# Kernel optimization log

Measured on AMD Instinct MI355X. Metric: run time of the kernel, lower is better.

## Reference

```python
import jax, jax.numpy as jnp
import numpy as np

HEADS = 4  # from init_kwargs

def setup_inputs() -> dict:
    key = jax.random.key(0)
    ks = jax.random.split(key, 11)
    B, N, T, E = 1, 16, 2048, 64
    D = E // HEADS
    return {
        "value": jax.random.normal(ks[0], (B, N, T, E), jnp.float32),
        "key":   jax.random.normal(ks[1], (B, N, T, E), jnp.float32),
        "query": jax.random.normal(ks[2], (B, N, T, E), jnp.float32),
        "Wq": jax.random.normal(ks[3], (D, D), jnp.float32) / np.sqrt(D),
        "bq": jax.random.normal(ks[4], (D,), jnp.float32) * 0.01,
        "Wk": jax.random.normal(ks[5], (D, D), jnp.float32) / np.sqrt(D),
        "bk": jax.random.normal(ks[6], (D,), jnp.float32) * 0.01,
        "Wv": jax.random.normal(ks[7], (D, D), jnp.float32) / np.sqrt(D),
        "bv": jax.random.normal(ks[8], (D,), jnp.float32) * 0.01,
        "Wfc": jax.random.normal(ks[9], (E, E), jnp.float32) / np.sqrt(E),
        "bfc": jax.random.normal(ks[10], (E,), jnp.float32) * 0.01,
    }

def reference(value, key, query, Wq, bq, Wk, bk, Wv, bv, Wfc, bfc):
    B, N, T, E = query.shape
    H = HEADS
    D = E // H
    # split heads: [B,N,T,H,D]
    q = query.reshape(B, N, T, H, D) @ Wq + bq
    k = key.reshape(B, N, T, H, D) @ Wk + bk
    v = value.reshape(B, N, T, H, D) @ Wv + bv
    # full score tensor [B,N,Tq,Tk,H]
    scores = jnp.einsum('bnqhd,bnkhd->bnqkh', q, k)
    # NOTE: original softmaxes over dim=2, i.e. the QUERY axis (faithful to source)
    attn = jax.nn.softmax(scores / jnp.float32(E) ** 0.5, axis=2)
    out = jnp.einsum('bnqkh,bnkhd->bnqhd', attn, v).reshape(B, N, T, E)
    return out @ Wfc + bfc
```

## Files before the change

kernel.cpp:

```cpp
#include <hip/hip_runtime.h>

#define N_ 16
#define T_ 2048
#define E_ 64
#define H_ 4
#define D_ 16
#define NH_ 64
#define SEXP_ 0.18033688f

typedef __attribute__((ext_vector_type(4))) _Float16 h4;
typedef __attribute__((ext_vector_type(8))) _Float16 h8;
typedef __attribute__((ext_vector_type(2))) __fp16 g2;
typedef __attribute__((ext_vector_type(4))) float f4;

#if __has_builtin(__builtin_amdgcn_exp2f)
__device__ inline float fast_exp2(float x) { return __builtin_amdgcn_exp2f(x); }
#else
__device__ inline float fast_exp2(float x) {
    float r; asm("v_exp_f32 %0, %1" : "=v"(r) : "v"(x)); return r;
}
#endif

#if __has_builtin(__builtin_amdgcn_rcpf)
__device__ inline float fast_rcp(float x) { return __builtin_amdgcn_rcpf(x); }
#else
__device__ inline float fast_rcp(float x) {
    float r; asm("v_rcp_f32 %0, %1" : "=v"(r) : "v"(x)); return r;
}
#endif

__device__ inline h4 pack4_f16(float a, float b, float c, float d) {
    union { g2 g[2]; h4 h; } u;
    u.g[0] = __builtin_amdgcn_cvt_pkrtz(a, b);
    u.g[1] = __builtin_amdgcn_cvt_pkrtz(c, d);
    return u.h;
}

__global__ __launch_bounds__(256) void proj_kernel(
    const float* __restrict__ xq, const float* __restrict__ Wq, const float* __restrict__ bq,
    const float* __restrict__ xk, const float* __restrict__ Wk, const float* __restrict__ bk,
    const float* __restrict__ xv, const float* __restrict__ Wv, const float* __restrict__ bv,
    const float* __restrict__ Wfc,
    _Float16* __restrict__ Qh, _Float16* __restrict__ Kh, _Float16* __restrict__ Vt,
    _Float16* __restrict__ Wt)
{
    int tid = threadIdx.x;
    int y = blockIdx.y;
    if (y == 3) {
        if (blockIdx.x < 16) {
            int k = blockIdx.x * 4 + (tid >> 6);
            int e = tid & 63;
            Wt[e * 64 + k] = (_Float16)Wfc[k * 64 + e];
        }
        return;
    }
    const float* x = (y == 0) ? xq : (y == 1) ? xk : xv;
    const float* W = (y == 0) ? Wq : (y == 1) ? Wk : Wv;
    const float* b = (y == 0) ? bq : (y == 1) ? bk : bv;
    const float sc = (y == 0) ? SEXP_ : 1.0f;

    __shared__ float Wl[D_ * D_];
    __shared__ float bl[D_];
    Wl[tid] = W[tid];
    if (tid < D_) bl[tid] = b[tid];
    __syncthreads();

    int r = blockIdx.x * 256 + tid;
    int h, t, n;
    if (y == 2) {
        t = r & (T_ - 1);
        h = (r >> 11) & (H_ - 1);
        n = r >> 13;
    } else {
        h = r & (H_ - 1);
        t = (r >> 2) & (T_ - 1);
        n = r >> 13;
    }

    const float4* xp4 = reinterpret_cast<const float4*>(
        x + ((size_t)(n * T_ + t) * E_ + h * D_));
    float xv_[D_];
#pragma unroll
    for (int i = 0; i < 4; i++) {
        float4 v = xp4[i];
        xv_[4*i] = v.x; xv_[4*i+1] = v.y; xv_[4*i+2] = v.z; xv_[4*i+3] = v.w;
    }
    float acc[D_];
#pragma unroll
    for (int i = 0; i < D_; i++) acc[i] = bl[i];
#pragma unroll
    for (int j = 0; j < D_; j++) {
        float xj = xv_[j];
#pragma unroll
        for (int i = 0; i < D_; i++) acc[i] = fmaf(xj, Wl[j * D_ + i], acc[i]);
    }
    if (y == 2) {
        _Float16* vb = Vt + (size_t)(n * H_ + h) * D_ * T_ + t;
#pragma unroll
        for (int d = 0; d < D_; d++) vb[(size_t)d * T_] = (_Float16)acc[d];
    } else {
        _Float16 ob[16];
#pragma unroll
        for (int i = 0; i < D_; i++) ob[i] = (_Float16)(acc[i] * sc);
        _Float16* o = (y == 0) ? Qh : Kh;
        uint4* dst = reinterpret_cast<uint4*>(o + (size_t)((n * H_ + h) * T_ + t) * D_);
        dst[0] = reinterpret_cast<uint4*>(ob)[0];
        dst[1] = reinterpret_cast<uint4*>(ob)[1];
    }
}

__global__ __attribute__((amdgpu_flat_work_group_size(1024, 1024)))
           __attribute__((amdgpu_waves_per_eu(4, 4)))
void fused_attn_kernel(
    const _Float16* __restrict__ Qh, const _Float16* __restrict__ Kh,
    const _Float16* __restrict__ Vt, float* __restrict__ PO)
{
    __shared__ __align__(16) _Float16 Qs[16 * 64 * 16];
    __shared__ __align__(16) float l[3][16];
    int tid = threadIdx.x;
    int lane = tid & 63, wave = tid >> 6;
    int row = lane & 15, quad = lane >> 4;
    int nh = blockIdx.x;
    int z = blockIdx.y;
    int k_lo = z * (T_ / 4);

    const _Float16* Kb = Kh + (size_t)nh * T_ * D_;
    const _Float16* Qb = Qh + (size_t)nh * T_ * D_;
    const _Float16* Vb = Vt + (size_t)nh * D_ * T_ + (size_t)row * T_;

    if (tid < 48) ((float*)l)[tid] = 0.f;

    {
        const uint4* src = reinterpret_cast<const uint4*>(Qb);
        uint4* dst = reinterpret_cast<uint4*>(Qs);
#pragma unroll
        for (int s = 0; s < 2; s++) {
            int u = tid * 2 + s;
            int w = u >> 7, rem = u & 127;
            int jrow = rem >> 1, half = rem & 1;
            dst[u] = src[(w * 128 + jrow) * 2 + half];
        }
    }

    h4 b2[4];
#pragma unroll
    for (int j = 0; j < 4; j++)
        b2[j] = *reinterpret_cast<const h4*>(Qb + ((wave * 8 + 4 + j) * 16 + row) * D_ + quad * 4);

    f4 o[8];
#pragma unroll
    for (int j = 0; j < 8; j++) o[j] = (f4){0.f, 0.f, 0.f, 0.f};
    f4 z4 = {0.f, 0.f, 0.f, 0.f};

    h4 a = *reinterpret_cast<const h4*>(Kb + (k_lo + row) * D_ + quad * 4);

    __syncthreads();

    const _Float16* QsW = Qs + wave * 1024;
    int cur = 0;
#pragma unroll 1
    for (int c = 0; c < 32; c++) {
        int k0 = k_lo + c * 16;
        h4 v = *reinterpret_cast<const h4*>(Vb + k0 + quad * 4);

        h4 p[8];
        f4 lp = {0.f, 0.f, 0.f, 0.f};

#pragma unroll
        for (int j = 0; j < 8; j++) {
            h4 bj = (j < 4)
                ? *reinterpret_cast<const h4*>(QsW + (j * 16 + row) * 16 + quad * 4)
                : b2[j - 4];
            f4 s = __builtin_amdgcn_mfma_f32_16x16x16f16(a, bj, z4, 0, 0, 0);
            float e0 = fast_exp2(s[0]), e1 = fast_exp2(s[1]),
                  e2 = fast_exp2(s[2]), e3 = fast_exp2(s[3]);
            lp[0] += e0; lp[1] += e1; lp[2] += e2; lp[3] += e3;
            p[j] = pack4_f16(e0, e1, e2, e3);
        }

        int kn = (c == 31) ? k_lo : k0 + 16;
        h4 na = *reinterpret_cast<const h4*>(Kb + (kn + row) * D_ + quad * 4);

#pragma unroll
        for (int off = 1; off < 16; off <<= 1) {
            lp[0] += __shfl_xor(lp[0], off, 64);
            lp[1] += __shfl_xor(lp[1], off, 64);
            lp[2] += __shfl_xor(lp[2], off, 64);
            lp[3] += __shfl_xor(lp[3], off, 64);
        }
        if (row == 0) {
#pragma unroll
            for (int i = 0; i < 4; i++) atomicAdd(&l[cur][quad * 4 + i], lp[i]);
        }
        __syncthreads();

        int zb = cur + 2; if (zb >= 3) zb -= 3;
        if (wave == 0 && lane < 16) l[zb][lane] = 0.f;

        f4 la = *reinterpret_cast<f4*>(&l[cur][quad * 4]);
        h4 rk;
        {
            union { g2 g[2]; h4 h; } u;
            u.g[0] = __builtin_amdgcn_cvt_pkrtz(fast_rcp(la[0]), fast_rcp(la[1]));
            u.g[1] = __builtin_amdgcn_cvt_pkrtz(fast_rcp(la[2]), fast_rcp(la[3]));
            rk = u.h;
        }
        h4 vs = v * rk;

#pragma unroll
        for (int j = 0; j < 8; j++)
            o[j] = __builtin_amdgcn_mfma_f32_16x16x16f16(p[j], vs, o[j], 0, 0, 0);

        a = na;
        cur = cur + 1; if (cur >= 3) cur -= 3;
    }

    int n = nh >> 2, h = nh & 3;
    float* po = PO + (size_t)z * N_ * T_ * E_ + (size_t)n * T_ * E_ + h * D_ + row;
#pragma unroll
    for (int j = 0; j < 8; j++)
#pragma unroll
        for (int i = 0; i < 4; i++) {
            int q0 = (wave * 8 + j) * 16 + quad * 4 + i;
            po[(size_t)q0 * E_] = o[j][i];
        }
}

__global__ __launch_bounds__(256) void fc_kernel(
    const float* __restrict__ PO, const _Float16* __restrict__ Wt,
    const float* __restrict__ bfc, float* __restrict__ out)
{
    int tid = threadIdx.x;
    int lane = tid & 63, wave = tid >> 6;
    int row = lane & 15, quad = lane >> 4;
    int g = blockIdx.x * 4 + wave;
    int r0 = g * 16;
    size_t base = (size_t)(r0 + row) * E_;
    const size_t zstride = (size_t)N_ * T_ * E_ / 4;

    h8 a[2];
#pragma unroll
    for (int half = 0; half < 2; half++) {
        f4 u0 = {0.f,0.f,0.f,0.f}, u1 = {0.f,0.f,0.f,0.f};
#pragma unroll
        for (int zz = 0; zz < 4; zz++) {
            const f4* p = reinterpret_cast<const f4*>(PO) + zz * zstride + base / 4;
            f4 w0 = p[half * 8 + quad * 2];
            f4 w1 = p[half * 8 + quad * 2 + 1];
#pragma unroll
            for (int i = 0; i < 4; i++) { u0[i] += w0[i]; u1[i] += w1[i]; }
        }
        union { h4 h[2]; h8 v; } pk;
        pk.h[0] = pack4_f16(u0[0], u0[1], u0[2], u0[3]);
        pk.h[1] = pack4_f16(u1[0], u1[1], u1[2], u1[3]);
        a[half] = pk.v;
    }
    f4 acc[4];
#pragma unroll
    for (int ne = 0; ne < 4; ne++) {
        const _Float16* wtb = Wt + (size_t)(ne * 16 + row) * 64;
        h8 b0 = *reinterpret_cast<const h8*>(wtb + quad * 8);
        h8 b1 = *reinterpret_cast<const h8*>(wtb + 32 + quad * 8);
        acc[ne] = __builtin_amdgcn_mfma_f32_16x16x32_f16(a[0], b0, (f4){0.f,0.f,0.f,0.f}, 0, 0, 0);
        acc[ne] = __builtin_amdgcn_mfma_f32_16x16x32_f16(a[1], b1, acc[ne], 0, 0, 0);
    }
#pragma unroll
    for (int ne = 0; ne < 4; ne++) {
        float bias = bfc[ne * 16 + row];
#pragma unroll
        for (int i = 0; i < 4; i++)
            out[(size_t)(r0 + quad * 4 + i) * E_ + ne * 16 + row] = acc[ne][i] + bias;
    }
}

extern "C" void kernel_launch(void* const* d_in, const int* in_sizes, int n_in,
                              void* d_out, int out_size, void* d_ws, size_t ws_size,
                              hipStream_t stream) {
    (void)in_sizes; (void)n_in; (void)out_size; (void)ws_size;
    const float* value = (const float*)d_in[0];
    const float* key   = (const float*)d_in[1];
    const float* query = (const float*)d_in[2];
    const float* Wq    = (const float*)d_in[3];
    const float* bq    = (const float*)d_in[4];
    const float* Wk    = (const float*)d_in[5];
    const float* bk    = (const float*)d_in[6];
    const float* Wv    = (const float*)d_in[7];
    const float* bv    = (const float*)d_in[8];
    const float* Wfc   = (const float*)d_in[9];
    const float* bfc   = (const float*)d_in[10];
    float* out = (float*)d_out;

    char* ws = (char*)d_ws;
    _Float16* Qh  = (_Float16*)(ws);
    _Float16* Kh  = (_Float16*)(ws + (4u << 20));
    _Float16* Vt  = (_Float16*)(ws + (8u << 20));
    _Float16* Wt  = (_Float16*)(ws + (12u << 20));
    float*    PO  = (float*)   (ws + (15u << 20));

    proj_kernel<<<dim3(512, 4), 256, 0, stream>>>(
        query, Wq, bq, key, Wk, bk, value, Wv, bv, Wfc, Qh, Kh, Vt, Wt);
    fused_attn_kernel<<<dim3(NH_, 4), 1024, 0, stream>>>(Qh, Kh, Vt, PO);
    fc_kernel<<<512, 256, 0, stream>>>(PO, Wt, bfc, out);
}
```

Measured before the change: 162.6 us.

## Software-pipeline score and PV phases, pad Q in LDS, use ds_swizzle reductions

Restructures the attention loop so the score/exp phase of chunk c overlaps with the PV MFMA of chunk c-1, using double-buffered P registers and a rotating triple of softmax-denominator buffers. With one barrier per iteration, the wait on the cross-wave column-sum reduction is taken off the critical path. All of Q is now staged in LDS with a padded stride of 20 halves to avoid bank conflicts, which replaces the previous register-held half. The shuffle-xor reductions become ds_swizzle. The cost is more LDS use and more live registers for the second P buffer, which may limit occupancy.

```diff
diff --git a/kernel.cpp b/kernel.cpp
--- a/kernel.cpp
+++ b/kernel.cpp
@@ -109,13 +109,63 @@
     }
 }
 
+#define S_PHASE(PD) do {                                                      \
+    lp = (f4){0.f, 0.f, 0.f, 0.f};                                            \
+    _Pragma("unroll")                                                         \
+    for (int j = 0; j < 8; j++) {                                             \
+        h4 bj = *reinterpret_cast<const h4*>(QsW + (j * 16 + row) * 20 + quad * 4); \
+        f4 s = __builtin_amdgcn_mfma_f32_16x16x16f16(a, bj, z4, 0, 0, 0);     \
+        float e0 = fast_exp2(s[0]), e1 = fast_exp2(s[1]);                     \
+        float e2 = fast_exp2(s[2]), e3 = fast_exp2(s[3]);                     \
+        lp[0] += e0; lp[1] += e1; lp[2] += e2; lp[3] += e3;                   \
+        PD[j] = pack4_f16(e0, e1, e2, e3);                                    \
+    }                                                                         \
+} while (0)
+
+#define SWZ_STEP(M)                                                           \
+    lp[0] += __int_as_float(__builtin_amdgcn_ds_swizzle(__float_as_int(lp[0]), M)); \
+    lp[1] += __int_as_float(__builtin_amdgcn_ds_swizzle(__float_as_int(lp[1]), M)); \
+    lp[2] += __int_as_float(__builtin_amdgcn_ds_swizzle(__float_as_int(lp[2]), M)); \
+    lp[3] += __int_as_float(__builtin_amdgcn_ds_swizzle(__float_as_int(lp[3]), M));
+
+#define REDUCE(BDST) do {                                                     \
+    SWZ_STEP(0x041F) SWZ_STEP(0x081F) SWZ_STEP(0x101F) SWZ_STEP(0x201F)       \
+    if (row == 0) {                                                           \
+        _Pragma("unroll")                                                     \
+        for (int i = 0; i < 4; i++) atomicAdd(&l[BDST][quad * 4 + i], lp[i]); \
+    }                                                                         \
+} while (0)
+
+#define ITER(C, PS, PPV, KN) do {                                             \
+    int k0 = k_lo + (C) * 16;                                                 \
+    h4 v = *reinterpret_cast<const h4*>(Vb + (k0 - 16) + quad * 4);           \
+    f4 la = *reinterpret_cast<f4*>(&l[bm1][quad * 4]);                        \
+    S_PHASE(PS);                                                              \
+    h4 na = *reinterpret_cast<const h4*>(Kb + ((KN) + row) * D_ + quad * 4);  \
+    REDUCE(b0);                                                               \
+    {                                                                         \
+        union { g2 g[2]; h4 h; } u_;                                          \
+        u_.g[0] = __builtin_amdgcn_cvt_pkrtz(fast_rcp(la[0]), fast_rcp(la[1])); \
+        u_.g[1] = __builtin_amdgcn_cvt_pkrtz(fast_rcp(la[2]), fast_rcp(la[3])); \
+        v = v * u_.h;                                                         \
+    }                                                                         \
+    _Pragma("unroll")                                                         \
+    for (int j = 0; j < 8; j++)                                               \
+        o[j] = __builtin_amdgcn_mfma_f32_16x16x16f16(PPV[j], v, o[j], 0, 0, 0); \
+    if (wave == 0 && lane < 16) l[bp1][lane] = 0.f;                           \
+    __syncthreads();                                                          \
+    a = na;                                                                   \
+} while (0)
+
+#define ROT() do { int t_ = bm1; bm1 = b0; b0 = bp1; bp1 = t_; } while (0)
+
 __global__ __attribute__((amdgpu_flat_work_group_size(1024, 1024)))
            __attribute__((amdgpu_waves_per_eu(4, 4)))
 void fused_attn_kernel(
     const _Float16* __restrict__ Qh, const _Float16* __restrict__ Kh,
     const _Float16* __restrict__ Vt, float* __restrict__ PO)
 {
-    __shared__ __align__(16) _Float16 Qs[16 * 64 * 16];
+    __shared__ __align__(16) _Float16 Qs[16 * 128 * 20];
     __shared__ __align__(16) float l[3][16];
     int tid = threadIdx.x;
     int lane = tid & 63, wave = tid >> 6;
@@ -131,21 +181,15 @@
     if (tid < 48) ((float*)l)[tid] = 0.f;
 
     {
-        const uint4* src = reinterpret_cast<const uint4*>(Qb);
-        uint4* dst = reinterpret_cast<uint4*>(Qs);
-#pragma unroll
-        for (int s = 0; s < 2; s++) {
-            int u = tid * 2 + s;
-            int w = u >> 7, rem = u & 127;
-            int jrow = rem >> 1, half = rem & 1;
-            dst[u] = src[(w * 128 + jrow) * 2 + half];
+        const uint2* src = reinterpret_cast<const uint2*>(Qb);
+        uint2* dq = reinterpret_cast<uint2*>(Qs);
+#pragma unroll
+        for (int s = 0; s < 8; s++) {
+            int u = s * 1024 + tid;
+            dq[(u >> 2) * 5 + (u & 3)] = src[u];
         }
     }
-
-    h4 b2[4];
-#pragma unroll
-    for (int j = 0; j < 4; j++)
-        b2[j] = *reinterpret_cast<const h4*>(Qb + ((wave * 8 + 4 + j) * 16 + row) * D_ + quad * 4);
+    const _Float16* QsW = Qs + wave * (128 * 20);
 
     f4 o[8];
 #pragma unroll
@@ -153,66 +197,40 @@
     f4 z4 = {0.f, 0.f, 0.f, 0.f};
 
     h4 a = *reinterpret_cast<const h4*>(Kb + (k_lo + row) * D_ + quad * 4);
+    h4 pA[8], pB[8];
+    f4 lp;
 
     __syncthreads();
 
-    const _Float16* QsW = Qs + wave * 1024;
-    int cur = 0;
+    S_PHASE(pA);
+    {
+        h4 na = *reinterpret_cast<const h4*>(Kb + (k_lo + 16 + row) * D_ + quad * 4);
+        REDUCE(0);
+        __syncthreads();
+        a = na;
+    }
+
+    int bm1 = 0, b0 = 1, bp1 = 2;
 #pragma unroll 1
-    for (int c = 0; c < 32; c++) {
-        int k0 = k_lo + c * 16;
-        h4 v = *reinterpret_cast<const h4*>(Vb + k0 + quad * 4);
-
-        h4 p[8];
-        f4 lp = {0.f, 0.f, 0.f, 0.f};
-
-#pragma unroll
-        for (int j = 0; j < 8; j++) {
-            h4 bj = (j < 4)
-                ? *reinterpret_cast<const h4*>(QsW + (j * 16 + row) * 16 + quad * 4)
-                : b2[j - 4];
-            f4 s = __builtin_amdgcn_mfma_f32_16x16x16f16(a, bj, z4, 0, 0, 0);
-            float e0 = fast_exp2(s[0]), e1 = fast_exp2(s[1]),
-                  e2 = fast_exp2(s[2]), e3 = fast_exp2(s[3]);
-            lp[0] += e0; lp[1] += e1; lp[2] += e2; lp[3] += e3;
-            p[j] = pack4_f16(e0, e1, e2, e3);
-        }
-
-        int kn = (c == 31) ? k_lo : k0 + 16;
-        h4 na = *reinterpret_cast<const h4*>(Kb + (kn + row) * D_ + quad * 4);
-
-#pragma unroll
-        for (int off = 1; off < 16; off <<= 1) {
-            lp[0] += __shfl_xor(lp[0], off, 64);
-            lp[1] += __shfl_xor(lp[1], off, 64);
-            lp[2] += __shfl_xor(lp[2], off, 64);
-            lp[3] += __shfl_xor(lp[3], off, 64);
-        }
-        if (row == 0) {
-#pragma unroll
-            for (int i = 0; i < 4; i++) atomicAdd(&l[cur][quad * 4 + i], lp[i]);
-        }
-        __syncthreads();
-
-        int zb = cur + 2; if (zb >= 3) zb -= 3;
-        if (wave == 0 && lane < 16) l[zb][lane] = 0.f;
-
-        f4 la = *reinterpret_cast<f4*>(&l[cur][quad * 4]);
-        h4 rk;
-        {
-            union { g2 g[2]; h4 h; } u;
-            u.g[0] = __builtin_amdgcn_cvt_pkrtz(fast_rcp(la[0]), fast_rcp(la[1]));
-            u.g[1] = __builtin_amdgcn_cvt_pkrtz(fast_rcp(la[2]), fast_rcp(la[3]));
-            rk = u.h;
-        }
-        h4 vs = v * rk;
-
+    for (int c = 1; c < 31; c += 2) {
+        ITER(c,     pB, pA, k_lo + c * 16 + 16);
+        ROT();
+        ITER(c + 1, pA, pB, k_lo + c * 16 + 32);
+        ROT();
+    }
+    ITER(31, pB, pA, k_lo);
+    ROT();
+
+    {
+        h4 v = *reinterpret_cast<const h4*>(Vb + (k_lo + 31 * 16) + quad * 4);
+        f4 la = *reinterpret_cast<f4*>(&l[bm1][quad * 4]);
+        union { g2 g[2]; h4 h; } u_;
+        u_.g[0] = __builtin_amdgcn_cvt_pkrtz(fast_rcp(la[0]), fast_rcp(la[1]));
+        u_.g[1] = __builtin_amdgcn_cvt_pkrtz(fast_rcp(la[2]), fast_rcp(la[3]));
+        v = v * u_.h;
 #pragma unroll
         for (int j = 0; j < 8; j++)
-            o[j] = __builtin_amdgcn_mfma_f32_16x16x16f16(p[j], vs, o[j], 0, 0, 0);
-
-        a = na;
-        cur = cur + 1; if (cur >= 3) cur -= 3;
+            o[j] = __builtin_amdgcn_mfma_f32_16x16x16f16(pB[j], v, o[j], 0, 0, 0);
     }
 
     int n = nh >> 2, h = nh & 3;
```

Result: no change. 163.6 us (+0.6%).
